# Kernel tuning notes

Hardware: AMD Instinct MI355X
Metric: run time of the kernel (lower is better)

## Reference

```python
import jax, jax.numpy as jnp
import numpy as np

N, B, D_IN, D_OUT, E = 1024, 128, 64, 64, 16


def setup_inputs() -> dict:
    key = jax.random.key(0)
    k1, k2, k3, k4 = jax.random.split(key, 4)
    x = jax.random.normal(k1, (B, N, D_IN), dtype=jnp.float32)
    node_embeddings = jax.random.normal(k2, (N, E), dtype=jnp.float32)
    weights_pool = jax.random.normal(k3, (E, D_IN, D_OUT), dtype=jnp.float32)
    bias_pool = jax.random.normal(k4, (E, D_OUT), dtype=jnp.float32)
    return {"x": x, "node_embeddings": node_embeddings,
            "weights_pool": weights_pool, "bias_pool": bias_pool}


def reference(x, node_embeddings, weights_pool, bias_pool):
    # Adaptive adjacency: softmax over rows of relu(E E^T), shape [N, N]
    scores = jax.nn.relu(node_embeddings @ node_embeddings.T)
    supports = jax.nn.softmax(scores, axis=1)
    # Per-node weights [N, D_IN, D_OUT] and bias [N, D_OUT]
    weights = jnp.einsum('nd,dio->nio', node_embeddings, weights_pool)
    bias = node_embeddings @ bias_pool  # [N, D_OUT]
    # Graph aggregation: [B, N, D_IN]
    x_g = jnp.einsum('nm,bmc->bnc', supports, x)
    # Per-node linear transform + bias: [B, N, D_OUT]
    x_gconv = jnp.einsum('bni,nio->bno', x_g, weights) + bias
    return x_gconv
```

## Files before the change

### kernel.cpp

```cpp
#include <hip/hip_runtime.h>

#define N_NODES 1024
#define BATCH   128
#define E_DIM   16


typedef __attribute__((ext_vector_type(8))) short bf16x8;
typedef __attribute__((ext_vector_type(4))) float f32x4;
typedef __attribute__((ext_vector_type(16))) float f32x16;

__device__ __forceinline__ unsigned short f2bf(float f) {
    union { float f; unsigned int u; } v; v.f = f;
    unsigned int u = v.u;
    u += 0x7FFFu + ((u >> 16) & 1u);
    return (unsigned short)(u >> 16);
}

__device__ __forceinline__ void gload_lds16(const void* g, void* l) {
    __builtin_amdgcn_global_load_lds(
        (const __attribute__((address_space(1))) unsigned int*)g,
        (__attribute__((address_space(3))) unsigned int*)l, 16, 0, 0);
}

__global__ __launch_bounds__(256) void k_prep2(const float* __restrict__ x,
                                               const float* __restrict__ emb,
                                               const float* __restrict__ wpool,
                                               const float* __restrict__ bpool,
                                               unsigned short* __restrict__ xbt,
                                               unsigned short* __restrict__ sup,
                                               unsigned short* __restrict__ Wt,
                                               float* __restrict__ bias) {
    __shared__ float sm[132];
    const int bid = blockIdx.x;
    const int t = threadIdx.x;

    if (bid < 2048) {
        const int b = bid >> 4, kt64 = bid & 15;
        unsigned short* dstp = xbt + (long)(b >> 1) * 131072 + kt64 * 8192
                             + (b & 1) * 512;
#pragma unroll
        for (int h = 0; h < 2; ++h) {
            const int g = h * 256 + t;
            const int kblk = g >> 6, c = g & 63;
            const float* s = x + ((long)b * 1024 + kt64 * 64 + kblk * 8) * 64 + c;
            bf16x8 r;
#pragma unroll
            for (int e = 0; e < 8; ++e) r[e] = (short)f2bf(s[e * 64]);
            *(bf16x8*)(dstp + kblk * 1024 + c * 8) = r;
        }
    } else if (bid < 2304) {
        float (*en4)[E_DIM] = (float(*)[E_DIM])sm;
        const int n0 = (bid - 2048) * 4;
        if (t < 64) en4[t >> 4][t & 15] = emb[(n0 + (t >> 4)) * E_DIM + (t & 15)];
        __syncthreads();
        const int o = t & 63;
#pragma unroll
        for (int p = 0; p < 2; ++p) {
            const int kblk = p * 4 + (t >> 6);
            float w[4][8];
#pragma unroll
            for (int nn = 0; nn < 4; ++nn)
#pragma unroll
                for (int e = 0; e < 8; ++e) w[nn][e] = 0.f;
            for (int ed = 0; ed < E_DIM; ++ed) {
                float v[8];
#pragma unroll
                for (int e = 0; e < 8; ++e)
                    v[e] = wpool[ed * 4096 + (kblk * 8 + e) * 64 + o];
#pragma unroll
                for (int nn = 0; nn < 4; ++nn)
#pragma unroll
                    for (int e = 0; e < 8; ++e)
                        w[nn][e] = fmaf(en4[nn][ed], v[e], w[nn][e]);
            }
#pragma unroll
            for (int nn = 0; nn < 4; ++nn) {
                bf16x8 r;
#pragma unroll
                for (int e = 0; e < 8; ++e) r[e] = (short)f2bf(w[nn][e]);
                *(bf16x8*)(Wt + (long)(n0 + nn) * 4096 + kblk * 512 + o * 8) = r;
            }
        }
        {
            const int nn = t >> 6, oo = t & 63;
            float s = 0.f;
#pragma unroll
            for (int e = 0; e < E_DIM; ++e) s = fmaf(en4[nn][e], bpool[e * 64 + oo], s);
            bias[(n0 + nn) * 64 + oo] = s;
        }
    } else {
        float* en  = sm;
        float* red = sm + 128;
        const int n = bid - 2304;
        if (t < E_DIM) en[t] = emb[n * E_DIM + t];
        __syncthreads();
        float sc[4];
        float mx = -1e30f;
#pragma unroll
        for (int r = 0; r < 4; ++r) {
            const float* em = &emb[(r * 256 + t) * E_DIM];
            float s = 0.f;
#pragma unroll
            for (int e = 0; e < E_DIM; ++e) s = fmaf(en[e], em[e], s);
            s = fmaxf(s, 0.f);
            sc[r] = s;
            mx = fmaxf(mx, s);
        }
#pragma unroll
        for (int o = 32; o > 0; o >>= 1) mx = fmaxf(mx, __shfl_xor(mx, o));
        if ((t & 63) == 0) red[t >> 6] = mx;
        __syncthreads();
        mx = fmaxf(fmaxf(red[0], red[1]), fmaxf(red[2], red[3]));
        float sum = 0.f;
#pragma unroll
        for (int r = 0; r < 4; ++r) { sc[r] = __expf(sc[r] - mx); sum += sc[r]; }
#pragma unroll
        for (int o = 32; o > 0; o >>= 1) sum += __shfl_xor(sum, o);
        __syncthreads();
        if ((t & 63) == 0) red[t >> 6] = sum;
        __syncthreads();
        sum = red[0] + red[1] + red[2] + red[3];
        const float inv = 1.f / sum;
#pragma unroll
        for (int r = 0; r < 4; ++r) {
            const int m = r * 256 + t;
            const int off = (n >> 7) * 131072 + (m >> 6) * 8192 + ((m >> 3) & 7) * 1024
                          + (n & 127) * 8 + (m & 7);
            sup[off] = f2bf(sc[r] * inv);
        }
    }
}

__global__ __launch_bounds__(256, 3) void k_agg(const unsigned short* __restrict__ S,
                                                const unsigned short* __restrict__ Bt,
                                                unsigned short* __restrict__ xg) {
    __shared__ __align__(16) char lds[49152];
    const int t = threadIdx.x;
    const int lane = t & 63, wid = t >> 6;

    const int hw   = blockIdx.x + 8 * blockIdx.y;
    const int work = (hw & 7) * 64 + (hw >> 3);
    const int n0 = (work & 7) * 128, j0 = (work >> 3) * 128;
    const int wr = wid >> 1, wc = wid & 1;

    f32x16 acc[2][2];
#pragma unroll
    for (int m = 0; m < 2; ++m)
#pragma unroll
        for (int n = 0; n < 2; ++n)
#pragma unroll
            for (int r = 0; r < 16; ++r) acc[m][n][r] = 0.f;

    const unsigned short* pA = S  + (n0 >> 7) * 131072 + lane * 8;
    const unsigned short* pB = Bt + (j0 >> 7) * 131072 + lane * 8;
    const unsigned short* sp[4];
    int doff[4];
#pragma unroll
    for (int i = 0; i < 4; ++i) {
        const int c = wid * 4 + i;
        if (c < 8) { sp[i] = pA + c * 512;       doff[i] = c * 1024; }
        else       { sp[i] = pB + (c - 8) * 512; doff[i] = 8192 + (c - 8) * 1024; }
    }
#define STAGE(bufidx, kt) do {                                           \
        char* buf_ = lds + (bufidx) * 16384;                             \
        const int ko_ = (kt) * 4096;                                     \
        gload_lds16(sp[0] + ko_, buf_ + doff[0]);                        \
        gload_lds16(sp[1] + ko_, buf_ + doff[1]);                        \
        gload_lds16(sp[2] + ko_, buf_ + doff[2]);                        \
        gload_lds16(sp[3] + ko_, buf_ + doff[3]);                        \
    } while (0)

    int aoff[2], boff[2];
#pragma unroll
    for (int m = 0; m < 2; ++m)
        aoff[m] = (lane >> 5) * 2048 + (wr * 64 + m * 32 + (lane & 31)) * 16;
#pragma unroll
    for (int n = 0; n < 2; ++n)
        boff[n] = 8192 + (lane >> 5) * 2048 + (wc * 64 + n * 32 + (lane & 31)) * 16;

    STAGE(0, 0); STAGE(1, 1);
    int bcur = 0;
    for (int kt = 0; kt < 32; ++kt) {
        if (kt < 31) asm volatile("s_waitcnt vmcnt(4)" ::: "memory");
        else         asm volatile("s_waitcnt vmcnt(0)" ::: "memory");
        __builtin_amdgcn_s_barrier();
        asm volatile("" ::: "memory");
        __builtin_amdgcn_sched_barrier(0);
        const int bprev = (bcur + 2 >= 3) ? bcur - 1 : bcur + 2;
        if (kt + 2 < 32) STAGE(bprev, kt + 2);
        const char* cur = lds + bcur * 16384;
        __builtin_amdgcn_s_setprio(1);
#pragma unroll
        for (int s = 0; s < 2; ++s) {
            bf16x8 a[2], b[2];
#pragma unroll
            for (int m = 0; m < 2; ++m) a[m] = *(const bf16x8*)(cur + s * 4096 + aoff[m]);
#pragma unroll
            for (int n = 0; n < 2; ++n) b[n] = *(const bf16x8*)(cur + s * 4096 + boff[n]);
#pragma unroll
            for (int m = 0; m < 2; ++m)
#pragma unroll
                for (int n = 0; n < 2; ++n)
                    acc[m][n] = __builtin_amdgcn_mfma_f32_32x32x16_bf16(a[m], b[n], acc[m][n], 0, 0, 0);
        }
        __builtin_amdgcn_s_setprio(0);
        asm volatile("" ::: "memory");
        __builtin_amdgcn_sched_barrier(0);
        bcur = (bcur + 1 >= 3) ? 0 : bcur + 1;
    }
#undef STAGE
    __syncthreads();

    char* lb = lds;
#pragma unroll
    for (int m = 0; m < 2; ++m) {
#pragma unroll
        for (int n = 0; n < 2; ++n) {
            const int col  = wc * 64 + n * 32 + (lane & 31);
            const int rowb = wr * 64 + m * 32 + 4 * (lane >> 5);
#pragma unroll
            for (int r = 0; r < 16; ++r) {
                const int row = rowb + (r & 3) + 8 * (r >> 2);
                *(unsigned short*)(lb + row * 256 + ((col * 2) ^ ((row & 7) << 4))) =
                    f2bf(acc[m][n][r]);
            }
        }
    }
    __syncthreads();
    const int b0 = j0 >> 6;
#pragma unroll
    for (int i = 0; i < 8; ++i) {
        const int idx = i * 256 + t;
        const int row = idx >> 4, cc = idx & 15;
        bf16x8 v = *(const bf16x8*)(lb + row * 256 + ((cc * 16) ^ ((row & 7) << 4)));
        const int b = b0 + (cc >> 3);
        const long dst = (long)(n0 + row) * 8192 + b * 64 + ((cc & 7) ^ (b & 7)) * 8;
        *(bf16x8*)(xg + dst) = v;
    }
}

__global__ __launch_bounds__(256) void k_out(const unsigned short* __restrict__ xg,
                                             const unsigned short* __restrict__ Wt,
                                             const float* __restrict__ bias,
                                             float* __restrict__ out) {
    __shared__ __align__(16) char lds[49152];
    const int t = threadIdx.x, lane = t & 63, wid = t >> 6;
    const int nb = blockIdx.x * 2;
#pragma unroll
    for (int i = 0; i < 12; ++i) {
        const int c = wid * 12 + i;
        if (c < 32) {
            const int nn = c >> 4, k = c & 15;
            gload_lds16(xg + (long)(nb + nn) * 8192 + k * 512 + lane * 8,
                        lds + nn * 16384 + k * 1024);
        } else {
            const int cc = c - 32, nn = cc >> 3, k = cc & 7;
            gload_lds16(Wt + (long)(nb + nn) * 4096 + k * 512 + lane * 8,
                        lds + 32768 + nn * 8192 + k * 1024);
        }
    }
    __syncthreads();

    const int ns   = wid >> 1;
    const int node = nb + ns;
    const int bh   = wid & 1;
    const char* xl  = lds + ns * 16384;
    const char* wlp = lds + 32768 + ns * 8192;
    const int p = lane & 15, q = lane >> 4;

    f32x4 acc[4][4];
#pragma unroll
    for (int m = 0; m < 4; ++m)
#pragma unroll
        for (int n = 0; n < 4; ++n) acc[m][n] = f32x4{0.f, 0.f, 0.f, 0.f};

#pragma unroll
    for (int s = 0; s < 2; ++s) {
        const int kb = s * 4 + q;
        bf16x8 a[4], b[4];
#pragma unroll
        for (int m = 0; m < 4; ++m) {
            const int brow = bh * 64 + m * 16 + p;
            a[m] = *(const bf16x8*)(xl + brow * 128 + ((kb ^ (lane & 7)) << 4));
        }
#pragma unroll
        for (int n = 0; n < 4; ++n)
            b[n] = *(const bf16x8*)(wlp + kb * 1024 + (n * 16 + p) * 16);
#pragma unroll
        for (int m = 0; m < 4; ++m)
#pragma unroll
            for (int n = 0; n < 4; ++n)
                acc[m][n] = __builtin_amdgcn_mfma_f32_16x16x32_bf16(a[m], b[n], acc[m][n], 0, 0, 0);
    }

    float bv[4];
#pragma unroll
    for (int n = 0; n < 4; ++n) bv[n] = bias[node * 64 + n * 16 + p];
    __syncthreads();

#pragma unroll
    for (int pass = 0; pass < 2; ++pass) {
        if (bh == pass) {
            char* tb = lds + ns * 17408;
#pragma unroll
            for (int m = 0; m < 4; ++m)
#pragma unroll
                for (int n = 0; n < 4; ++n)
#pragma unroll
                    for (int r = 0; r < 4; ++r) {
                        const int brow = m * 16 + q * 4 + r;
                        *(float*)(tb + brow * 272 + (n * 16 + p) * 4) =
                            acc[m][n][r] + bv[n];
                    }
        }
        __syncthreads();
#pragma unroll
        for (int i = 0; i < 8; ++i) {
            const int idx = i * 256 + t;
            const int tns = idx >> 10, rem = idx & 1023;
            const int b = rem >> 4, g = rem & 15;
            f32x4 v = *(const f32x4*)(lds + tns * 17408 + b * 272 + g * 16);
            *(f32x4*)(out + (long)(pass * 64 + b) * 65536 + (nb + tns) * 64 + g * 4) = v;
        }
        __syncthreads();
    }
}

extern "C" void kernel_launch(void* const* d_in, const int* in_sizes, int n_in,
                              void* d_out, int out_size, void* d_ws, size_t ws_size,
                              hipStream_t stream) {
    const float* x     = (const float*)d_in[0];
    const float* emb   = (const float*)d_in[1];
    const float* wpool = (const float*)d_in[2];
    const float* bpool = (const float*)d_in[3];
    float* out = (float*)d_out;

    char* ws = (char*)d_ws;
    unsigned short* sup  = (unsigned short*)(ws);
    unsigned short* xbt  = (unsigned short*)(ws + (2u  << 20));
    unsigned short* Wt   = (unsigned short*)(ws + (18u << 20));
    float*          bias = (float*)         (ws + (26u << 20));
    unsigned short* xg   = (unsigned short*)(ws + (27u << 20));
    (void)in_sizes; (void)n_in; (void)out_size; (void)ws_size;

    k_prep2<<<dim3(3328), dim3(256), 0, stream>>>(x, emb, wpool, bpool,
                                                  xbt, sup, Wt, bias);
    k_agg<<<dim3(8, 64), dim3(256), 0, stream>>>(sup, xbt, xg);
    k_out<<<dim3(512), dim3(256), 0, stream>>>(xg, Wt, bias, out);
}
```

Measured before the change: 55.51 us.

## Enlarge k_agg output tile to 128x256 so each wave computes 128x64

The aggregation GEMM tile grows from 128x128 to 128x256 columns. Each wave now owns a 128x64 strip with 4x2 MFMA accumulators instead of 2x2, so every A fragment loaded from LDS is reused across more outputs. The grid is halved to 256 blocks, LDS per block grows to 72KB with a three-stage buffer, and occupancy drops to 2 blocks per CU. The epilogue writes the results back in two passes through LDS, which adds barriers. With 256 blocks on a 256-CU device, this risks leaving parallelism unused.

```diff
diff --git a/kernel.cpp b/kernel.cpp
--- a/kernel.cpp
+++ b/kernel.cpp
@@ -131,74 +131,83 @@
     }
 }
 
-__global__ __launch_bounds__(256, 3) void k_agg(const unsigned short* __restrict__ S,
+__global__ __launch_bounds__(256, 2) void k_agg(const unsigned short* __restrict__ S,
                                                 const unsigned short* __restrict__ Bt,
                                                 unsigned short* __restrict__ xg) {
-    __shared__ __align__(16) char lds[49152];
+    __shared__ __align__(16) char lds[73728];
     const int t = threadIdx.x;
     const int lane = t & 63, wid = t >> 6;
 
-    const int hw   = blockIdx.x + 8 * blockIdx.y;
-    const int work = (hw & 7) * 64 + (hw >> 3);
-    const int n0 = (work & 7) * 128, j0 = (work >> 3) * 128;
-    const int wr = wid >> 1, wc = wid & 1;
-
-    f32x16 acc[2][2];
-#pragma unroll
-    for (int m = 0; m < 2; ++m)
+    const int hw   = blockIdx.x;
+    const int work = (hw & 7) * 32 + (hw >> 3);
+    const int n0 = (work & 7) * 128, j0 = (work >> 3) * 256;
+
+    f32x16 acc[4][2];
+#pragma unroll
+    for (int m = 0; m < 4; ++m)
 #pragma unroll
         for (int n = 0; n < 2; ++n)
 #pragma unroll
             for (int r = 0; r < 16; ++r) acc[m][n][r] = 0.f;
 
-    const unsigned short* pA = S  + (n0 >> 7) * 131072 + lane * 8;
-    const unsigned short* pB = Bt + (j0 >> 7) * 131072 + lane * 8;
-    const unsigned short* sp[4];
-    int doff[4];
-#pragma unroll
-    for (int i = 0; i < 4; ++i) {
-        const int c = wid * 4 + i;
-        if (c < 8) { sp[i] = pA + c * 512;       doff[i] = c * 1024; }
-        else       { sp[i] = pB + (c - 8) * 512; doff[i] = 8192 + (c - 8) * 1024; }
+    const unsigned short* sp[6];
+    int doff[6];
+#pragma unroll
+    for (int i = 0; i < 6; ++i) {
+        const int c = wid * 6 + i;
+        if (c < 8) {
+            sp[i]   = S + (n0 >> 7) * 131072 + c * 512 + lane * 8;
+            doff[i] = c * 1024;
+        } else {
+            const int cc = c - 8;
+            sp[i]   = Bt + (long)((j0 >> 7) + (cc >> 3)) * 131072
+                    + (cc & 7) * 512 + lane * 8;
+            doff[i] = 8192 + cc * 1024;
+        }
     }
 #define STAGE(bufidx, kt) do {                                           \
-        char* buf_ = lds + (bufidx) * 16384;                             \
+        char* buf_ = lds + (bufidx) * 24576;                             \
         const int ko_ = (kt) * 4096;                                     \
         gload_lds16(sp[0] + ko_, buf_ + doff[0]);                        \
         gload_lds16(sp[1] + ko_, buf_ + doff[1]);                        \
         gload_lds16(sp[2] + ko_, buf_ + doff[2]);                        \
         gload_lds16(sp[3] + ko_, buf_ + doff[3]);                        \
+        gload_lds16(sp[4] + ko_, buf_ + doff[4]);                        \
+        gload_lds16(sp[5] + ko_, buf_ + doff[5]);                        \
     } while (0)
 
-    int aoff[2], boff[2];
-#pragma unroll
-    for (int m = 0; m < 2; ++m)
-        aoff[m] = (lane >> 5) * 2048 + (wr * 64 + m * 32 + (lane & 31)) * 16;
-#pragma unroll
-    for (int n = 0; n < 2; ++n)
-        boff[n] = 8192 + (lane >> 5) * 2048 + (wc * 64 + n * 32 + (lane & 31)) * 16;
+    const int lh = lane >> 5, lr = lane & 31;
+    int aoff[4], boff[2];
+#pragma unroll
+    for (int m = 0; m < 4; ++m)
+        aoff[m] = lh * 2048 + (m * 32 + lr) * 16;
+#pragma unroll
+    for (int n = 0; n < 2; ++n) {
+        const int jcol = wid * 64 + n * 32 + lr;
+        boff[n] = 8192 + (jcol >> 7) * 8192 + lh * 2048 + (jcol & 127) * 16;
+    }
 
     STAGE(0, 0); STAGE(1, 1);
     int bcur = 0;
     for (int kt = 0; kt < 32; ++kt) {
-        if (kt < 31) asm volatile("s_waitcnt vmcnt(4)" ::: "memory");
+        if (kt < 31) asm volatile("s_waitcnt vmcnt(6)" ::: "memory");
         else         asm volatile("s_waitcnt vmcnt(0)" ::: "memory");
         __builtin_amdgcn_s_barrier();
         asm volatile("" ::: "memory");
         __builtin_amdgcn_sched_barrier(0);
         const int bprev = (bcur + 2 >= 3) ? bcur - 1 : bcur + 2;
         if (kt + 2 < 32) STAGE(bprev, kt + 2);
-        const char* cur = lds + bcur * 16384;
+        const char* cur = lds + bcur * 24576;
         __builtin_amdgcn_s_setprio(1);
 #pragma unroll
         for (int s = 0; s < 2; ++s) {
-            bf16x8 a[2], b[2];
-#pragma unroll
-            for (int m = 0; m < 2; ++m) a[m] = *(const bf16x8*)(cur + s * 4096 + aoff[m]);
+            bf16x8 a[4], b[2];
+#pragma unroll
+            for (int m = 0; m < 4; ++m) a[m] = *(const bf16x8*)(cur + s * 4096 + aoff[m]);
 #pragma unroll
             for (int n = 0; n < 2; ++n) b[n] = *(const bf16x8*)(cur + s * 4096 + boff[n]);
 #pragma unroll
-            for (int m = 0; m < 2; ++m)
+            for (int m = 0; m < 4; ++m)
 #pragma unroll
                 for (int n = 0; n < 2; ++n)
                     acc[m][n] = __builtin_amdgcn_mfma_f32_32x32x16_bf16(a[m], b[n], acc[m][n], 0, 0, 0);
@@ -212,30 +221,37 @@
     __syncthreads();
 
     char* lb = lds;
-#pragma unroll
-    for (int m = 0; m < 2; ++m) {
-#pragma unroll
-        for (int n = 0; n < 2; ++n) {
-            const int col  = wc * 64 + n * 32 + (lane & 31);
-            const int rowb = wr * 64 + m * 32 + 4 * (lane >> 5);
-#pragma unroll
-            for (int r = 0; r < 16; ++r) {
-                const int row = rowb + (r & 3) + 8 * (r >> 2);
-                *(unsigned short*)(lb + row * 256 + ((col * 2) ^ ((row & 7) << 4))) =
-                    f2bf(acc[m][n][r]);
+    const int b0base = j0 >> 6;
+#pragma unroll
+    for (int pass = 0; pass < 2; ++pass) {
+        if ((wid >> 1) == pass) {
+            const int colb = (wid & 1) * 64;
+#pragma unroll
+            for (int m = 0; m < 4; ++m) {
+                const int rowb = m * 32 + 4 * lh;
+#pragma unroll
+                for (int n = 0; n < 2; ++n) {
+                    const int col = colb + n * 32 + lr;
+#pragma unroll
+                    for (int r = 0; r < 16; ++r) {
+                        const int row = rowb + (r & 3) + 8 * (r >> 2);
+                        *(unsigned short*)(lb + row * 256 + ((col * 2) ^ ((row & 7) << 4))) =
+                            f2bf(acc[m][n][r]);
+                    }
+                }
             }
         }
-    }
-    __syncthreads();
-    const int b0 = j0 >> 6;
-#pragma unroll
-    for (int i = 0; i < 8; ++i) {
-        const int idx = i * 256 + t;
-        const int row = idx >> 4, cc = idx & 15;
-        bf16x8 v = *(const bf16x8*)(lb + row * 256 + ((cc * 16) ^ ((row & 7) << 4)));
-        const int b = b0 + (cc >> 3);
-        const long dst = (long)(n0 + row) * 8192 + b * 64 + ((cc & 7) ^ (b & 7)) * 8;
-        *(bf16x8*)(xg + dst) = v;
+        __syncthreads();
+#pragma unroll
+        for (int i = 0; i < 8; ++i) {
+            const int idx = i * 256 + t;
+            const int row = idx >> 4, cc = idx & 15;
+            bf16x8 v = *(const bf16x8*)(lb + row * 256 + ((cc * 16) ^ ((row & 7) << 4)));
+            const int b = b0base + pass * 2 + (cc >> 3);
+            const long dst = (long)(n0 + row) * 8192 + b * 64 + ((cc & 7) ^ (b & 7)) * 8;
+            *(bf16x8*)(xg + dst) = v;
+        }
+        __syncthreads();
     }
 }
 
@@ -345,6 +361,6 @@
 
     k_prep2<<<dim3(3328), dim3(256), 0, stream>>>(x, emb, wpool, bpool,
                                                   xbt, sup, Wt, bias);
-    k_agg<<<dim3(8, 64), dim3(256), 0, stream>>>(sup, xbt, xg);
+    k_agg<<<dim3(256), dim3(256), 0, stream>>>(sup, xbt, xg);
     k_out<<<dim3(512), dim3(256), 0, stream>>>(xg, Wt, bias, out);
 }
```

Result: slower. 57.84 us (+4.2%).

## Enlarge aggregation GEMM tile to 256x128 with 8 waves per block

Applied to the files above, without the earlier changes.

The aggregation GEMM block tile grows from 128x128 to 256 node rows by 128 columns. Blocks now have 512 threads (8 waves), the grid shrinks to 256 blocks, and each wave issues 3 async global-to-LDS loads per stage instead of 4. The goal is better reuse of the B (x) tile across more rows and less total global traffic per output. In exchange the kernel uses more LDS (72KB triple buffer), drops to fewer resident blocks per CU, and with 256 blocks there may be only about one wave of blocks on 256 CUs.

```diff
diff --git a/kernel.cpp b/kernel.cpp
--- a/kernel.cpp
+++ b/kernel.cpp
@@ -131,18 +131,18 @@
     }
 }
 
-__global__ __launch_bounds__(256, 3) void k_agg(const unsigned short* __restrict__ S,
+__global__ __launch_bounds__(512, 2) void k_agg(const unsigned short* __restrict__ S,
                                                 const unsigned short* __restrict__ Bt,
                                                 unsigned short* __restrict__ xg) {
-    __shared__ __align__(16) char lds[49152];
+    __shared__ __align__(16) char lds[73728];
     const int t = threadIdx.x;
     const int lane = t & 63, wid = t >> 6;
-
-    const int hw   = blockIdx.x + 8 * blockIdx.y;
-    const int work = (hw & 7) * 64 + (hw >> 3);
-    const int n0 = (work & 7) * 128, j0 = (work >> 3) * 128;
     const int wr = wid >> 1, wc = wid & 1;
 
+    const int hw   = blockIdx.x;
+    const int work = (hw & 7) * 32 + (hw >> 3);
+    const int n0 = (work & 3) * 256, j0 = (work >> 2) * 128;
+
     f32x16 acc[2][2];
 #pragma unroll
     for (int m = 0; m < 2; ++m)
@@ -151,44 +151,53 @@
 #pragma unroll
             for (int r = 0; r < 16; ++r) acc[m][n][r] = 0.f;
 
-    const unsigned short* pA = S  + (n0 >> 7) * 131072 + lane * 8;
-    const unsigned short* pB = Bt + (j0 >> 7) * 131072 + lane * 8;
-    const unsigned short* sp[4];
-    int doff[4];
-#pragma unroll
-    for (int i = 0; i < 4; ++i) {
-        const int c = wid * 4 + i;
-        if (c < 8) { sp[i] = pA + c * 512;       doff[i] = c * 1024; }
-        else       { sp[i] = pB + (c - 8) * 512; doff[i] = 8192 + (c - 8) * 1024; }
+    const unsigned short* sp[3];
+    int doff[3];
+#pragma unroll
+    for (int i = 0; i < 3; ++i) {
+        const int c = wid * 3 + i;
+        if (c < 16) {
+            const int p = c >> 3, ch = c & 7;
+            sp[i]   = S + (long)((n0 >> 7) + p) * 131072 + ch * 512 + lane * 8;
+            doff[i] = p * 8192 + ch * 1024;
+        } else {
+            const int ch = c - 16;
+            sp[i]   = Bt + (long)(j0 >> 7) * 131072 + ch * 512 + lane * 8;
+            doff[i] = 16384 + ch * 1024;
+        }
     }
 #define STAGE(bufidx, kt) do {                                           \
-        char* buf_ = lds + (bufidx) * 16384;                             \
+        char* buf_ = lds + (bufidx) * 24576;                             \
         const int ko_ = (kt) * 4096;                                     \
         gload_lds16(sp[0] + ko_, buf_ + doff[0]);                        \
         gload_lds16(sp[1] + ko_, buf_ + doff[1]);                        \
         gload_lds16(sp[2] + ko_, buf_ + doff[2]);                        \
-        gload_lds16(sp[3] + ko_, buf_ + doff[3]);                        \
     } while (0)
 
+    const int lh = lane >> 5, lr = lane & 31;
     int aoff[2], boff[2];
 #pragma unroll
-    for (int m = 0; m < 2; ++m)
-        aoff[m] = (lane >> 5) * 2048 + (wr * 64 + m * 32 + (lane & 31)) * 16;
-#pragma unroll
-    for (int n = 0; n < 2; ++n)
-        boff[n] = 8192 + (lane >> 5) * 2048 + (wc * 64 + n * 32 + (lane & 31)) * 16;
+    for (int m = 0; m < 2; ++m) {
+        const int row = wr * 64 + m * 32 + lr;
+        aoff[m] = (row >> 7) * 8192 + lh * 2048 + (row & 127) * 16;
+    }
+#pragma unroll
+    for (int n = 0; n < 2; ++n) {
+        const int jcol = wc * 64 + n * 32 + lr;
+        boff[n] = 16384 + lh * 2048 + jcol * 16;
+    }
 
     STAGE(0, 0); STAGE(1, 1);
     int bcur = 0;
     for (int kt = 0; kt < 32; ++kt) {
-        if (kt < 31) asm volatile("s_waitcnt vmcnt(4)" ::: "memory");
+        if (kt < 31) asm volatile("s_waitcnt vmcnt(3)" ::: "memory");
         else         asm volatile("s_waitcnt vmcnt(0)" ::: "memory");
         __builtin_amdgcn_s_barrier();
         asm volatile("" ::: "memory");
         __builtin_amdgcn_sched_barrier(0);
         const int bprev = (bcur + 2 >= 3) ? bcur - 1 : bcur + 2;
         if (kt + 2 < 32) STAGE(bprev, kt + 2);
-        const char* cur = lds + bcur * 16384;
+        const char* cur = lds + bcur * 24576;
         __builtin_amdgcn_s_setprio(1);
 #pragma unroll
         for (int s = 0; s < 2; ++s) {
@@ -214,10 +223,10 @@
     char* lb = lds;
 #pragma unroll
     for (int m = 0; m < 2; ++m) {
+        const int rowb = wr * 64 + m * 32 + 4 * lh;
 #pragma unroll
         for (int n = 0; n < 2; ++n) {
-            const int col  = wc * 64 + n * 32 + (lane & 31);
-            const int rowb = wr * 64 + m * 32 + 4 * (lane >> 5);
+            const int col = wc * 64 + n * 32 + lr;
 #pragma unroll
             for (int r = 0; r < 16; ++r) {
                 const int row = rowb + (r & 3) + 8 * (r >> 2);
@@ -230,7 +239,7 @@
     const int b0 = j0 >> 6;
 #pragma unroll
     for (int i = 0; i < 8; ++i) {
-        const int idx = i * 256 + t;
+        const int idx = i * 512 + t;
         const int row = idx >> 4, cc = idx & 15;
         bf16x8 v = *(const bf16x8*)(lb + row * 256 + ((cc * 16) ^ ((row & 7) << 4)));
         const int b = b0 + (cc >> 3);
@@ -345,6 +354,6 @@
 
     k_prep2<<<dim3(3328), dim3(256), 0, stream>>>(x, emb, wpool, bpool,
                                                   xbt, sup, Wt, bias);
-    k_agg<<<dim3(8, 64), dim3(256), 0, stream>>>(sup, xbt, xg);
+    k_agg<<<dim3(256), dim3(512), 0, stream>>>(sup, xbt, xg);
     k_out<<<dim3(512), dim3(256), 0, stream>>>(xg, Wt, bias, out);
 }
```

Result: no change. 56.60 us (+2.0%).
